# Optimization experiments

Hardware: AMD Instinct MI355X
Metric: run time of the kernel (lower is better)

## Reference

```python
import jax, jax.numpy as jnp
import numpy as np

NUM_HEADS = 8
TOP_K = 32
LN_EPS = 1e-5
RENORM_EPS = 1e-5


def _split_heads(x):
    # [B, S, D] -> [B, H, S, d]
    B, S, D = x.shape
    return x.reshape(B, S, NUM_HEADS, D // NUM_HEADS).transpose(0, 2, 1, 3)


def setup_inputs() -> dict:
    key = jax.random.key(0)
    k1, k2, k3, k4 = jax.random.split(key, 4)
    B, S, D, H = 2, 2048, 1024, NUM_HEADS
    q = jax.random.normal(k1, (B, S, D), dtype=jnp.float32)
    k = jax.random.normal(k2, (B, S, D), dtype=jnp.float32)
    v = jax.random.normal(k3, (B, S, D), dtype=jnp.float32)
    attention_weight = jax.random.normal(k4, (B, H, S, S), dtype=jnp.float32)
    gamma = jnp.ones((D,), dtype=jnp.float32)
    beta = jnp.zeros((D,), dtype=jnp.float32)
    return {"q": q, "k": k, "v": v, "attention_weight": attention_weight,
            "gamma": gamma, "beta": beta}


def reference(q, k, v, attention_weight, gamma, beta):
    B, S, D = q.shape
    qh = _split_heads(q)  # [B,H,S,d]
    kh = _split_heads(k)
    vh = _split_heads(v)
    # Unscaled QK^T (faithful to source: no /sqrt(d))
    scores = jnp.einsum("bhqd,bhkd->bhqk", qh, kh)
    probs = jax.nn.softmax(scores, axis=-1)
    # top-k mask via double argsort: rank of each key by descending weight
    rank = jnp.argsort(jnp.argsort(-attention_weight, axis=-1), axis=-1)
    top_mask = (rank < TOP_K).astype(probs.dtype)
    probs = probs * top_mask
    probs = probs / (jnp.sum(probs, axis=-1, keepdims=True) + RENORM_EPS)
    out = jnp.einsum("bhqk,bhkd->bhqd", probs, vh)
    out = out.transpose(0, 2, 1, 3).reshape(B, S, D)
    # LayerNorm over last dim
    mu = jnp.mean(out, axis=-1, keepdims=True)
    var = jnp.var(out, axis=-1, keepdims=True)
    out = (out - mu) * jax.lax.rsqrt(var + LN_EPS) * gamma + beta
    return out
```

## Files before the change

kernel.cpp:

```cpp
#include <hip/hip_runtime.h>
#include <hip/hip_bf16.h>
#include <stdint.h>

#define BB 2
#define SS 2048
#define DD 1024
#define HH 8
#define HD 128
#define TOPK 32
#define ROWS (BB*HH*SS)

__global__ __launch_bounds__(256) void topk_kernel(const float* __restrict__ aw,
                                                   int* __restrict__ idx_out) {
    const int row = blockIdx.x;
    const float* p = aw + (size_t)row * SS;
    const int t = threadIdx.x;
    float4 v0 = *(const float4*)(p + 4 * t);
    float4 v1 = *(const float4*)(p + 1024 + 4 * t);
    float vals[8] = {v0.x, v0.y, v0.z, v0.w, v1.x, v1.y, v1.z, v1.w};
    unsigned long long key[8];
#pragma unroll
    for (int i = 0; i < 8; i++) {
        int e = (i < 4) ? (4 * t + i) : (1024 + 4 * t + (i - 4));
        unsigned u = __float_as_uint(vals[i]);
        unsigned sk = (u & 0x80000000u) ? ~u : (u | 0x80000000u);
        key[i] = ((unsigned long long)sk << 11) | (unsigned)(2047 - e);
    }
    __shared__ int s_cnt;
    __shared__ int s_red[4];
    __shared__ unsigned long long s_cand[256];
    const int lane = t & 63, wv = t >> 6;

    unsigned thr0 = __float_as_uint(1.76f) | 0x80000000u;
    unsigned long long T = ((unsigned long long)thr0 << 11) | 2047ull;

    if (t == 0) s_cnt = 0;
    __syncthreads();
#pragma unroll
    for (int i = 0; i < 8; i++) {
        if (key[i] > T) {
            int pos = atomicAdd(&s_cnt, 1);
            if (pos < 256) s_cand[pos] = key[i];
        }
    }
    __syncthreads();

    if (s_cnt < TOPK || s_cnt > 256) {
        unsigned long long lo = 0, hi = ~0ull;
        if (s_cnt > 256) lo = T; else hi = T;
        T = lo + ((hi - lo) >> 1);
        for (int it = 0; it < 40; ++it) {
            int c = 0;
#pragma unroll
            for (int i = 0; i < 8; i++) c += (key[i] > T) ? 1 : 0;
            for (int off = 32; off; off >>= 1) c += __shfl_down(c, off, 64);
            if (lane == 0) s_red[wv] = c;
            __syncthreads();
            int tot = s_red[0] + s_red[1] + s_red[2] + s_red[3];
            if (tot >= TOPK && tot <= 256) break;
            if (tot > 256) lo = T; else hi = T;
            T = lo + ((hi - lo) >> 1);
            __syncthreads();
        }
        if (t == 0) s_cnt = 0;
        __syncthreads();
#pragma unroll
        for (int i = 0; i < 8; i++) {
            if (key[i] > T) {
                int pos = atomicAdd(&s_cnt, 1);
                if (pos < 256) s_cand[pos] = key[i];
            }
        }
        __syncthreads();
    }

    const int C = s_cnt < 256 ? s_cnt : 256;
    if (t < C) {
        unsigned long long mk = s_cand[t];
        int rank = 0;
        for (int j = 0; j < C; ++j)
            rank += (s_cand[j] > mk) ? 1 : 0;
        if (rank < TOPK)
            idx_out[(size_t)row * TOPK + rank] = 2047 - (int)(mk & 2047ull);
    }
}

typedef float f32x4 __attribute__((ext_vector_type(4)));
typedef _Float16 f16x8 __attribute__((ext_vector_type(8)));
typedef _Float16 f16x4 __attribute__((ext_vector_type(4)));

#define KPAD 136

__global__ __launch_bounds__(256) void stats_kernel(const float* __restrict__ q,
                                                    const float* __restrict__ k,
                                                    float* __restrict__ ws_m,
                                                    float* __restrict__ ws_l) {
    __shared__ __align__(16) _Float16 Qs[128 * KPAD];
    __shared__ __align__(16) _Float16 Ks[128 * KPAD];
    const int blk = blockIdx.x & 255;
    const int half = blockIdx.x >> 8;
    const int bh = blk >> 4;
    const int qt = blk & 15;
    const int b = bh >> 3, h = bh & 7;
    const int t = threadIdx.x;
    const int wv = t >> 6, lane = t & 63;
    const int l16 = lane & 15, quad = lane >> 4;

    const float* qbase = q + ((size_t)(b * SS + qt * 128) * DD + h * HD);
#pragma unroll
    for (int i = 0; i < 16; ++i) {
        int fi = t + 256 * i;
        int r = fi >> 5, c4 = fi & 31;
        float4 f = *(const float4*)(qbase + (size_t)r * DD + c4 * 4);
        *(f16x4*)&Qs[r * KPAD + c4 * 4] =
            (f16x4){(_Float16)f.x, (_Float16)f.y, (_Float16)f.z, (_Float16)f.w};
    }
    float mrun[2][4], lrun[2][4];
#pragma unroll
    for (int a = 0; a < 2; a++)
#pragma unroll
        for (int r2 = 0; r2 < 4; r2++) { mrun[a][r2] = -INFINITY; lrun[a][r2] = 0.f; }

    const float* kbase = k + ((size_t)(b * SS) * DD + h * HD);
    for (int kt = half * 8; kt < half * 8 + 8; ++kt) {
        __syncthreads();
#pragma unroll
        for (int i = 0; i < 16; ++i) {
            int fi = t + 256 * i;
            int r = fi >> 5, c4 = fi & 31;
            float4 f = *(const float4*)(kbase + (size_t)(kt * 128 + r) * DD + c4 * 4);
            *(f16x4*)&Ks[r * KPAD + c4 * 4] =
                (f16x4){(_Float16)f.x, (_Float16)f.y, (_Float16)f.z, (_Float16)f.w};
        }
        __syncthreads();
        f32x4 acc[2][8];
#pragma unroll
        for (int a = 0; a < 2; a++)
#pragma unroll
            for (int n = 0; n < 8; n++) acc[a][n] = (f32x4){0.f, 0.f, 0.f, 0.f};
#pragma unroll
        for (int ks = 0; ks < 4; ++ks) {
            f16x8 af[2], bfr[8];
#pragma unroll
            for (int a = 0; a < 2; a++)
                af[a] = *(const f16x8*)&Qs[(wv * 32 + a * 16 + l16) * KPAD + ks * 32 + quad * 8];
#pragma unroll
            for (int n = 0; n < 8; n++)
                bfr[n] = *(const f16x8*)&Ks[(n * 16 + l16) * KPAD + ks * 32 + quad * 8];
#pragma unroll
            for (int a = 0; a < 2; a++)
#pragma unroll
                for (int n = 0; n < 8; n++)
                    acc[a][n] = __builtin_amdgcn_mfma_f32_16x16x32_f16(af[a], bfr[n], acc[a][n], 0, 0, 0);
        }
#pragma unroll
        for (int a = 0; a < 2; a++) {
#pragma unroll
            for (int r2 = 0; r2 < 4; r2++) {
                float tm = acc[a][0][r2];
#pragma unroll
                for (int n = 1; n < 8; n++) tm = fmaxf(tm, acc[a][n][r2]);
#pragma unroll
                for (int off = 1; off < 16; off <<= 1) tm = fmaxf(tm, __shfl_xor(tm, off, 64));
                float tl = 0.f;
#pragma unroll
                for (int n = 0; n < 8; n++) tl += __expf(acc[a][n][r2] - tm);
#pragma unroll
                for (int off = 1; off < 16; off <<= 1) tl += __shfl_xor(tl, off, 64);
                float mo = mrun[a][r2];
                float mn = fmaxf(mo, tm);
                lrun[a][r2] = lrun[a][r2] * __expf(mo - mn) + tl * __expf(tm - mn);
                mrun[a][r2] = mn;
            }
        }
    }
    if (l16 == 0) {
#pragma unroll
        for (int a = 0; a < 2; a++)
#pragma unroll
            for (int r2 = 0; r2 < 4; r2++) {
                int rrow = qt * 128 + wv * 32 + a * 16 + quad * 4 + r2;
                size_t g = (size_t)half * ROWS + (size_t)bh * SS + rrow;
                ws_m[g] = mrun[a][r2];
                ws_l[g] = lrun[a][r2];
            }
    }
}

__global__ __launch_bounds__(128) void attnout_kernel(const float* __restrict__ q,
                                                      const float* __restrict__ k,
                                                      const float* __restrict__ v,
                                                      const int* __restrict__ idx_ws,
                                                      const float* __restrict__ ws_m,
                                                      const float* __restrict__ ws_l,
                                                      float* __restrict__ out) {
    const int bh = blockIdx.x & 15;
    const int s = blockIdx.x >> 4;
    const int R = (bh << 11) | s;
    const int b = bh >> 3, h = bh & 7;
    const int t = threadIdx.x;
    __shared__ float q_l[128];
    __shared__ int idx_l[32];
    __shared__ float e_l[32];
    __shared__ float w_l[32];
    const float* qrow = q + ((size_t)(b * SS + s) * DD + h * HD);
    q_l[t] = qrow[t];
    if (t < 32) idx_l[t] = idx_ws[(size_t)R * TOPK + t];
    __syncthreads();
    const float m0 = ws_m[R], m1 = ws_m[(size_t)ROWS + R];
    const float l0 = ws_l[R], l1 = ws_l[(size_t)ROWS + R];
    const float m = fmaxf(m0, m1);
    const float Z = l0 * __expf(m0 - m) + l1 * __expf(m1 - m);
    const int l32 = t & 31, g = t >> 5;
    float4 q4 = *(const float4*)&q_l[l32 * 4];
    const float* kb = k + ((size_t)b * SS * DD + h * HD);
#pragma unroll
    for (int p = 0; p < 8; ++p) {
        int i = p * 4 + g;
        int ki = idx_l[i];
        float4 kv = *(const float4*)(kb + (size_t)ki * DD + l32 * 4);
        float d = q4.x * kv.x + q4.y * kv.y + q4.z * kv.z + q4.w * kv.w;
#pragma unroll
        for (int off = 1; off < 32; off <<= 1) d += __shfl_xor(d, off, 64);
        if (l32 == 0) e_l[i] = __expf(d - m);
    }
    __syncthreads();
    if (t < 32) {
        float e = e_l[t];
        float ssum = e;
#pragma unroll
        for (int off = 1; off < 32; off <<= 1) ssum += __shfl_xor(ssum, off, 64);
        float den = ssum + 1e-5f * Z;
        w_l[t] = e / den;
    }
    __syncthreads();
    const float* vb = v + ((size_t)b * SS * DD + h * HD);
    float accv = 0.f;
#pragma unroll 8
    for (int i = 0; i < 32; ++i) {
        accv += w_l[i] * vb[(size_t)idx_l[i] * DD + t];
    }
    out[((size_t)(b * SS + s) * DD) + h * HD + t] = accv;
}

__global__ __launch_bounds__(256) void ln_kernel(float* __restrict__ out,
                                                 const float* __restrict__ gamma,
                                                 const float* __restrict__ beta) {
    const int row = blockIdx.x;
    float* p = out + (size_t)row * DD;
    const int t = threadIdx.x;
    float x[4];
#pragma unroll
    for (int i = 0; i < 4; i++) x[i] = p[t + 256 * i];
    float sum = x[0] + x[1] + x[2] + x[3];
    __shared__ float red[4];
    const int lane = t & 63, wv = t >> 6;
    for (int off = 32; off; off >>= 1) sum += __shfl_down(sum, off, 64);
    if (lane == 0) red[wv] = sum;
    __syncthreads();
    float mean = (red[0] + red[1] + red[2] + red[3]) * (1.f / DD);
    __syncthreads();
    float vs = 0.f;
#pragma unroll
    for (int i = 0; i < 4; i++) { float d = x[i] - mean; vs += d * d; }
    for (int off = 32; off; off >>= 1) vs += __shfl_down(vs, off, 64);
    if (lane == 0) red[wv] = vs;
    __syncthreads();
    float var = (red[0] + red[1] + red[2] + red[3]) * (1.f / DD);
    float inv = rsqrtf(var + 1e-5f);
#pragma unroll
    for (int i = 0; i < 4; i++) {
        int c = t + 256 * i;
        p[c] = (x[i] - mean) * inv * gamma[c] + beta[c];
    }
}

extern "C" void kernel_launch(void* const* d_in, const int* in_sizes, int n_in,
                              void* d_out, int out_size, void* d_ws, size_t ws_size,
                              hipStream_t stream) {
    const float* q = (const float*)d_in[0];
    const float* k = (const float*)d_in[1];
    const float* v = (const float*)d_in[2];
    const float* aw = (const float*)d_in[3];
    const float* gamma = (const float*)d_in[4];
    const float* beta = (const float*)d_in[5];
    float* out = (float*)d_out;

    int* idx_ws = (int*)d_ws;
    float* ws_m = (float*)((char*)d_ws + (size_t)ROWS * TOPK * sizeof(int));
    float* ws_l = ws_m + 2 * ROWS;

    hipLaunchKernelGGL(topk_kernel, dim3(ROWS), dim3(256), 0, stream, aw, idx_ws);
    hipLaunchKernelGGL(stats_kernel, dim3(512), dim3(256), 0, stream, q, k, ws_m, ws_l);
    hipLaunchKernelGGL(attnout_kernel, dim3(ROWS), dim3(128), 0, stream, q, k, v, idx_ws, ws_m, ws_l, out);
    hipLaunchKernelGGL(ln_kernel, dim3(BB * SS), dim3(256), 0, stream, out, gamma, beta);
}
```

Baseline: 531.4 us.

## Pre-convert Q/K/V to head-major fp16 and pipeline stats kernel with async LDS loads

Adds a conversion kernel that writes Q, K and V as fp16 in head-major layout. The stats kernel now reads those fp16 copies with global_load_lds into a swizzled, double-buffered K tile, keeps Q fragments in registers, and splits the key range into quarters so it launches twice as many blocks. The attention-output kernel gathers V from the fp16 copy with vectorized loads and reduces the partial sums through shared memory. The goal is less redundant fp32 traffic and conversion work in the QK pass, plus overlap of K loads with MFMA compute. The cost is an extra pass over Q, K and V and reduced V precision.

```diff
diff --git a/kernel.cpp b/kernel.cpp
--- a/kernel.cpp
+++ b/kernel.cpp
@@ -1,5 +1,4 @@
 #include <hip/hip_runtime.h>
-#include <hip/hip_bf16.h>
 #include <stdint.h>
 
 #define BB 2
@@ -9,6 +8,38 @@
 #define HD 128
 #define TOPK 32
 #define ROWS (BB*HH*SS)
+#define BH 16
+
+typedef float f32x4 __attribute__((ext_vector_type(4)));
+typedef _Float16 f16x8 __attribute__((ext_vector_type(8)));
+typedef _Float16 f16x4 __attribute__((ext_vector_type(4)));
+
+__device__ __forceinline__ void gload_lds16(const _Float16* g, _Float16* l) {
+    __builtin_amdgcn_global_load_lds(
+        (const __attribute__((address_space(1))) void*)g,
+        (__attribute__((address_space(3))) void*)l, 16, 0, 0);
+}
+
+__global__ __launch_bounds__(256) void cvt_kernel(const float* __restrict__ q,
+                                                  const float* __restrict__ k,
+                                                  const float* __restrict__ v,
+                                                  _Float16* __restrict__ q16,
+                                                  _Float16* __restrict__ k16,
+                                                  _Float16* __restrict__ v16) {
+    const int row = blockIdx.x;
+    const int b = row >> 11, s = row & 2047;
+    const int t = threadIdx.x;
+    const int h = t >> 5, d4 = (t & 31) * 4;
+    const size_t src = (size_t)row * DD + t * 4;
+    const size_t dst = ((size_t)(b * HH + h) * SS + s) * HD + d4;
+    float4 f;
+    f = *(const float4*)(q + src);
+    *(f16x4*)(q16 + dst) = (f16x4){(_Float16)f.x,(_Float16)f.y,(_Float16)f.z,(_Float16)f.w};
+    f = *(const float4*)(k + src);
+    *(f16x4*)(k16 + dst) = (f16x4){(_Float16)f.x,(_Float16)f.y,(_Float16)f.z,(_Float16)f.w};
+    f = *(const float4*)(v + src);
+    *(f16x4*)(v16 + dst) = (f16x4){(_Float16)f.x,(_Float16)f.y,(_Float16)f.z,(_Float16)f.w};
+}
 
 __global__ __launch_bounds__(256) void topk_kernel(const float* __restrict__ aw,
                                                    int* __restrict__ idx_out) {
@@ -85,86 +116,93 @@
     }
 }
 
-typedef float f32x4 __attribute__((ext_vector_type(4)));
-typedef _Float16 f16x8 __attribute__((ext_vector_type(8)));
-typedef _Float16 f16x4 __attribute__((ext_vector_type(4)));
-
-#define KPAD 136
-
-__global__ __launch_bounds__(256) void stats_kernel(const float* __restrict__ q,
-                                                    const float* __restrict__ k,
+__global__ __launch_bounds__(256) void stats_kernel(const _Float16* __restrict__ q16,
+                                                    const _Float16* __restrict__ k16,
                                                     float* __restrict__ ws_m,
                                                     float* __restrict__ ws_l) {
-    __shared__ __align__(16) _Float16 Qs[128 * KPAD];
-    __shared__ __align__(16) _Float16 Ks[128 * KPAD];
-    const int blk = blockIdx.x & 255;
-    const int half = blockIdx.x >> 8;
-    const int bh = blk >> 4;
-    const int qt = blk & 15;
-    const int b = bh >> 3, h = bh & 7;
+    __shared__ __align__(16) _Float16 Ks[2][64 * 128];
+    const int xcd = blockIdx.x & 7;
+    const int r = blockIdx.x >> 3;
+    const int bh = xcd * 2 + (r & 1);
+    const int rr = r >> 1;
+    const int qt = rr & 15;
+    const int quarter = rr >> 4;
     const int t = threadIdx.x;
     const int wv = t >> 6, lane = t & 63;
     const int l16 = lane & 15, quad = lane >> 4;
 
-    const float* qbase = q + ((size_t)(b * SS + qt * 128) * DD + h * HD);
-#pragma unroll
-    for (int i = 0; i < 16; ++i) {
-        int fi = t + 256 * i;
-        int r = fi >> 5, c4 = fi & 31;
-        float4 f = *(const float4*)(qbase + (size_t)r * DD + c4 * 4);
-        *(f16x4*)&Qs[r * KPAD + c4 * 4] =
-            (f16x4){(_Float16)f.x, (_Float16)f.y, (_Float16)f.z, (_Float16)f.w};
-    }
+    const _Float16* qb = q16 + ((size_t)bh * SS + qt * 128 + wv * 32 + l16) * HD;
+    f16x8 af[2][4];
+#pragma unroll
+    for (int a = 0; a < 2; a++)
+#pragma unroll
+        for (int ks = 0; ks < 4; ks++)
+            af[a][ks] = *(const f16x8*)(qb + a * 16 * HD + ks * 32 + quad * 8);
+
+    const int lr = lane >> 4, lc = lane & 15;
+    int srco[4];
+#pragma unroll
+    for (int i = 0; i < 4; i++) {
+        int x = ((i & 1) * 4) + lr;
+        srco[i] = (wv * 16 + i * 4 + lr) * HD + ((lc ^ x) * 8);
+    }
+    const _Float16* kb = k16 + (size_t)bh * SS * HD;
+
+    int rdoff[4];
+#pragma unroll
+    for (int ks = 0; ks < 4; ks++)
+        rdoff[ks] = (((ks * 4 + quad) ^ (l16 & 7)) * 8);
+
     float mrun[2][4], lrun[2][4];
 #pragma unroll
     for (int a = 0; a < 2; a++)
 #pragma unroll
         for (int r2 = 0; r2 < 4; r2++) { mrun[a][r2] = -INFINITY; lrun[a][r2] = 0.f; }
 
-    const float* kbase = k + ((size_t)(b * SS) * DD + h * HD);
-    for (int kt = half * 8; kt < half * 8 + 8; ++kt) {
-        __syncthreads();
-#pragma unroll
-        for (int i = 0; i < 16; ++i) {
-            int fi = t + 256 * i;
-            int r = fi >> 5, c4 = fi & 31;
-            float4 f = *(const float4*)(kbase + (size_t)(kt * 128 + r) * DD + c4 * 4);
-            *(f16x4*)&Ks[r * KPAD + c4 * 4] =
-                (f16x4){(_Float16)f.x, (_Float16)f.y, (_Float16)f.z, (_Float16)f.w};
-        }
-        __syncthreads();
-        f32x4 acc[2][8];
+    {
+        const _Float16* src = kb + (size_t)(quarter * 8) * 64 * HD;
+#pragma unroll
+        for (int i = 0; i < 4; i++)
+            gload_lds16(src + srco[i], &Ks[0][(wv * 4 + i) * 512]);
+    }
+    __syncthreads();
+
+    int cur = 0;
+    for (int tt = 0; tt < 8; ++tt) {
+        if (tt < 7) {
+            const _Float16* src = kb + (size_t)(quarter * 8 + tt + 1) * 64 * HD;
+#pragma unroll
+            for (int i = 0; i < 4; i++)
+                gload_lds16(src + srco[i], &Ks[cur ^ 1][(wv * 4 + i) * 512]);
+        }
+        f32x4 acc[2][4];
 #pragma unroll
         for (int a = 0; a < 2; a++)
 #pragma unroll
-            for (int n = 0; n < 8; n++) acc[a][n] = (f32x4){0.f, 0.f, 0.f, 0.f};
+            for (int n = 0; n < 4; n++) acc[a][n] = (f32x4){0.f, 0.f, 0.f, 0.f};
 #pragma unroll
         for (int ks = 0; ks < 4; ++ks) {
-            f16x8 af[2], bfr[8];
+            f16x8 bfr[4];
+#pragma unroll
+            for (int n = 0; n < 4; n++)
+                bfr[n] = *(const f16x8*)&Ks[cur][(n * 16 + l16) * HD + rdoff[ks]];
 #pragma unroll
             for (int a = 0; a < 2; a++)
-                af[a] = *(const f16x8*)&Qs[(wv * 32 + a * 16 + l16) * KPAD + ks * 32 + quad * 8];
-#pragma unroll
-            for (int n = 0; n < 8; n++)
-                bfr[n] = *(const f16x8*)&Ks[(n * 16 + l16) * KPAD + ks * 32 + quad * 8];
-#pragma unroll
-            for (int a = 0; a < 2; a++)
-#pragma unroll
-                for (int n = 0; n < 8; n++)
-                    acc[a][n] = __builtin_amdgcn_mfma_f32_16x16x32_f16(af[a], bfr[n], acc[a][n], 0, 0, 0);
+#pragma unroll
+                for (int n = 0; n < 4; n++)
+                    acc[a][n] = __builtin_amdgcn_mfma_f32_16x16x32_f16(af[a][ks], bfr[n], acc[a][n], 0, 0, 0);
         }
 #pragma unroll
         for (int a = 0; a < 2; a++) {
 #pragma unroll
             for (int r2 = 0; r2 < 4; r2++) {
-                float tm = acc[a][0][r2];
-#pragma unroll
-                for (int n = 1; n < 8; n++) tm = fmaxf(tm, acc[a][n][r2]);
+                float tm = fmaxf(fmaxf(acc[a][0][r2], acc[a][1][r2]),
+                                 fmaxf(acc[a][2][r2], acc[a][3][r2]));
 #pragma unroll
                 for (int off = 1; off < 16; off <<= 1) tm = fmaxf(tm, __shfl_xor(tm, off, 64));
                 float tl = 0.f;
 #pragma unroll
-                for (int n = 0; n < 8; n++) tl += __expf(acc[a][n][r2] - tm);
+                for (int n = 0; n < 4; n++) tl += __expf(acc[a][n][r2] - tm);
 #pragma unroll
                 for (int off = 1; off < 16; off <<= 1) tl += __shfl_xor(tl, off, 64);
                 float mo = mrun[a][r2];
@@ -173,14 +211,17 @@
                 mrun[a][r2] = mn;
             }
         }
-    }
+        __syncthreads();
+        cur ^= 1;
+    }
+
     if (l16 == 0) {
 #pragma unroll
         for (int a = 0; a < 2; a++)
 #pragma unroll
             for (int r2 = 0; r2 < 4; r2++) {
                 int rrow = qt * 128 + wv * 32 + a * 16 + quad * 4 + r2;
-                size_t g = (size_t)half * ROWS + (size_t)bh * SS + rrow;
+                size_t g = (size_t)quarter * ROWS + (size_t)bh * SS + rrow;
                 ws_m[g] = mrun[a][r2];
                 ws_l[g] = lrun[a][r2];
             }
@@ -189,7 +230,7 @@
 
 __global__ __launch_bounds__(128) void attnout_kernel(const float* __restrict__ q,
                                                       const float* __restrict__ k,
-                                                      const float* __restrict__ v,
+                                                      const _Float16* __restrict__ v16,
                                                       const int* __restrict__ idx_ws,
                                                       const float* __restrict__ ws_m,
                                                       const float* __restrict__ ws_l,
@@ -203,14 +244,20 @@
     __shared__ int idx_l[32];
     __shared__ float e_l[32];
     __shared__ float w_l[32];
+    __shared__ __align__(16) float s_pv[4][128];
     const float* qrow = q + ((size_t)(b * SS + s) * DD + h * HD);
     q_l[t] = qrow[t];
     if (t < 32) idx_l[t] = idx_ws[(size_t)R * TOPK + t];
     __syncthreads();
-    const float m0 = ws_m[R], m1 = ws_m[(size_t)ROWS + R];
-    const float l0 = ws_l[R], l1 = ws_l[(size_t)ROWS + R];
-    const float m = fmaxf(m0, m1);
-    const float Z = l0 * __expf(m0 - m) + l1 * __expf(m1 - m);
+    float m = ws_m[R];
+    m = fmaxf(m, ws_m[(size_t)ROWS + R]);
+    m = fmaxf(m, ws_m[2 * (size_t)ROWS + R]);
+    m = fmaxf(m, ws_m[3 * (size_t)ROWS + R]);
+    float Z = 0.f;
+#pragma unroll
+    for (int qr = 0; qr < 4; ++qr)
+        Z += ws_l[(size_t)qr * ROWS + R] * __expf(ws_m[(size_t)qr * ROWS + R] - m);
+
     const int l32 = t & 31, g = t >> 5;
     float4 q4 = *(const float4*)&q_l[l32 * 4];
     const float* kb = k + ((size_t)b * SS * DD + h * HD);
@@ -234,13 +281,22 @@
         w_l[t] = e / den;
     }
     __syncthreads();
-    const float* vb = v + ((size_t)b * SS * DD + h * HD);
-    float accv = 0.f;
-#pragma unroll 8
-    for (int i = 0; i < 32; ++i) {
-        accv += w_l[i] * vb[(size_t)idx_l[i] * DD + t];
-    }
-    out[((size_t)(b * SS + s) * DD) + h * HD + t] = accv;
+    const _Float16* vb = v16 + (size_t)bh * SS * HD;
+    float a0 = 0.f, a1 = 0.f, a2 = 0.f, a3 = 0.f;
+#pragma unroll
+    for (int p = 0; p < 8; ++p) {
+        int i = p * 4 + g;
+        f16x4 hv = *(const f16x4*)(vb + (size_t)idx_l[i] * HD + l32 * 4);
+        float w = w_l[i];
+        a0 += w * (float)hv[0];
+        a1 += w * (float)hv[1];
+        a2 += w * (float)hv[2];
+        a3 += w * (float)hv[3];
+    }
+    *(float4*)&s_pv[g][l32 * 4] = make_float4(a0, a1, a2, a3);
+    __syncthreads();
+    out[((size_t)(b * SS + s) * DD) + h * HD + t] =
+        s_pv[0][t] + s_pv[1][t] + s_pv[2][t] + s_pv[3][t];
 }
 
 __global__ __launch_bounds__(256) void ln_kernel(float* __restrict__ out,
@@ -287,11 +343,15 @@
     float* out = (float*)d_out;
 
     int* idx_ws = (int*)d_ws;
-    float* ws_m = (float*)((char*)d_ws + (size_t)ROWS * TOPK * sizeof(int));
-    float* ws_l = ws_m + 2 * ROWS;
-
+    float* ws_m = (float*)((char*)d_ws + ((size_t)4 << 20));
+    float* ws_l = ws_m + (size_t)4 * ROWS;
+    _Float16* q16 = (_Float16*)((char*)d_ws + ((size_t)8 << 20));
+    _Float16* k16 = q16 + (size_t)BH * SS * HD;
+    _Float16* v16 = k16 + (size_t)BH * SS * HD;
+
+    hipLaunchKernelGGL(cvt_kernel, dim3(BB * SS), dim3(256), 0, stream, q, k, v, q16, k16, v16);
     hipLaunchKernelGGL(topk_kernel, dim3(ROWS), dim3(256), 0, stream, aw, idx_ws);
-    hipLaunchKernelGGL(stats_kernel, dim3(512), dim3(256), 0, stream, q, k, ws_m, ws_l);
-    hipLaunchKernelGGL(attnout_kernel, dim3(ROWS), dim3(128), 0, stream, q, k, v, idx_ws, ws_m, ws_l, out);
+    hipLaunchKernelGGL(stats_kernel, dim3(1024), dim3(256), 0, stream, q16, k16, ws_m, ws_l);
+    hipLaunchKernelGGL(attnout_kernel, dim3(ROWS), dim3(128), 0, stream, q, k, v16, idx_ws, ws_m, ws_l, out);
     hipLaunchKernelGGL(ln_kernel, dim3(BB * SS), dim3(256), 0, stream, out, gamma, beta);
 }
```

Result: no change. 525.0 us (median of 2 runs) (-1.2%).
